# Performance work log

Measured on AMD Instinct MI355X. Metric: run time of the kernel, lower is better.

## Reference

```python
import jax, jax.numpy as jnp
import numpy as np

K = 32           # number of neighbors (init kwarg k)
NUM_CLASSES = 100  # fixed class vocabulary for jit-compatible bincount


def setup_inputs() -> dict:
    key = jax.random.key(0)
    k1, k2, k3 = jax.random.split(key, 3)
    X_test = jax.random.normal(k1, (2048, 512), dtype=jnp.float32)
    X_train = jax.random.normal(k2, (65536, 512), dtype=jnp.float32)
    y_train = jax.random.randint(k3, (65536,), 0, NUM_CLASSES, dtype=jnp.int32)
    return {"X_test": X_test, "X_train": X_train, "y_train": y_train}


def reference(X_test, X_train, y_train):
    # Pairwise euclidean distances via ||q||^2 - 2 q.t + ||t||^2  -> [Nq, Nt]
    q2 = jnp.sum(X_test * X_test, axis=1, keepdims=True)        # [Nq, 1]
    t2 = jnp.sum(X_train * X_train, axis=1)                      # [Nt]
    d2 = q2 - 2.0 * (X_test @ X_train.T) + t2[None, :]           # [Nq, Nt]
    dist = jnp.sqrt(jnp.maximum(d2, 0.0))
    # k smallest distances -> neighbor indices
    _, idx = jax.lax.top_k(-dist, K)                             # [Nq, K]
    neighbor_labels = y_train[idx]                               # [Nq, K]
    # bincount per query (vectorized) + argmax = majority vote
    counts = jnp.sum(jax.nn.one_hot(neighbor_labels, NUM_CLASSES, dtype=jnp.float32), axis=1)  # [Nq, C]
    y_pred = jnp.argmax(counts, axis=1).astype(jnp.int32)        # [Nq]
    return y_pred
```

## Files before the change

kernel.cpp:

```cpp
#include <hip/hip_runtime.h>
#include <hip/hip_bf16.h>
#include <stdint.h>

typedef unsigned long long u64;
typedef unsigned int u32;
typedef unsigned short u16;
typedef __attribute__((ext_vector_type(8))) short short8;
typedef __attribute__((ext_vector_type(16))) float float16;

#define NQ 2048
#define NT 65536
#define DIM 512
#define KNN 32
#define NC 100
#define NS 32

#define QT 32
#define SLICE (NT / NS)
#define TT 256
#define KK 16
#define FCAP 32

#define PQT 32
#define PTT 256
#define PSLICE 512
#define NTPRE 2048

#define MQT 128
#define MTT 128
#define MBK 32
#define MSLICE 2048
#define SCAP 16
#define NTILES 256

#define GCAP 4096

__global__ void norm_kernel(const float* __restrict__ X, float* __restrict__ out, int nrows) {
    int row = blockIdx.x * 4 + (threadIdx.x >> 6);
    int lane = threadIdx.x & 63;
    if (row >= nrows) return;
    const float4* p = (const float4*)(X + (size_t)row * DIM);
    float4 a = p[lane];
    float4 b = p[lane + 64];
    float s = a.x*a.x + a.y*a.y + a.z*a.z + a.w*a.w
            + b.x*b.x + b.y*b.y + b.z*b.z + b.w*b.w;
    #pragma unroll
    for (int off = 32; off > 0; off >>= 1) s += __shfl_down(s, off, 64);
    if (lane == 0) out[row] = s;
}

__global__ void split_kernel(const float* __restrict__ X, u16* __restrict__ H,
                             u16* __restrict__ L, int n4) {
    int i = blockIdx.x * 256 + threadIdx.x;
    if (i >= n4) return;
    float4 v = ((const float4*)X)[i];
    float f[4] = {v.x, v.y, v.z, v.w};
    u16 hh[4], ll[4];
    #pragma unroll
    for (int j = 0; j < 4; ++j) {
        union { __hip_bfloat16 b; u16 u; } cv;
        cv.b = __float2bfloat16(f[j]);
        hh[j] = cv.u;
        float hf = __bfloat162float(cv.b);
        cv.b = __float2bfloat16(f[j] - hf);
        ll[j] = cv.u;
    }
    ((ushort4*)H)[i] = make_ushort4(hh[0], hh[1], hh[2], hh[3]);
    ((ushort4*)L)[i] = make_ushort4(ll[0], ll[1], ll[2], ll[3]);
}

__launch_bounds__(256, 2)
__global__ void knn_pre(const float* __restrict__ Xq, const float* __restrict__ Xt,
                        const float* __restrict__ q2, const float* __restrict__ t2,
                        float* __restrict__ Dpre) {
    __shared__ float sQ[KK][PQT];
    __shared__ float sT[KK][PTT];

    const int tid = threadIdx.x;
    const int q0 = blockIdx.x * PQT;
    const int t0p = blockIdx.y * PSLICE;
    const int tq4 = (tid >> 5) * 4;
    const int tt4 = (tid & 31) * 4;
    const int pg = tid & 63;
    const int kg = tid >> 6;
    const int qp = tid & 31;
    const int kq = tid >> 5;

    float qq[4];
    #pragma unroll
    for (int i = 0; i < 4; ++i) qq[i] = q2[q0 + tq4 + i];

    #pragma unroll 1
    for (int chunk = 0; chunk < PSLICE / PTT; ++chunk) {
        const int tbase = t0p + chunk * PTT;
        float acc[4][8];
        #pragma unroll
        for (int i = 0; i < 4; ++i)
            #pragma unroll
            for (int j = 0; j < 8; ++j) acc[i][j] = 0.f;

        #pragma unroll 1
        for (int k0 = 0; k0 < DIM; k0 += KK) {
            __syncthreads();
            {
                const float* Tp = Xt + (size_t)(tbase + pg * 4) * DIM + k0 + kg * 4;
                float4 r0 = *(const float4*)(Tp);
                float4 r1 = *(const float4*)(Tp + DIM);
                float4 r2 = *(const float4*)(Tp + 2 * DIM);
                float4 r3 = *(const float4*)(Tp + 3 * DIM);
                *(float4*)&sT[kg * 4 + 0][pg * 4] = make_float4(r0.x, r1.x, r2.x, r3.x);
                *(float4*)&sT[kg * 4 + 1][pg * 4] = make_float4(r0.y, r1.y, r2.y, r3.y);
                *(float4*)&sT[kg * 4 + 2][pg * 4] = make_float4(r0.z, r1.z, r2.z, r3.z);
                *(float4*)&sT[kg * 4 + 3][pg * 4] = make_float4(r0.w, r1.w, r2.w, r3.w);
            }
            {
                float2 v = *(const float2*)(Xq + (size_t)(q0 + qp) * DIM + k0 + kq * 2);
                sQ[kq * 2 + 0][qp] = v.x;
                sQ[kq * 2 + 1][qp] = v.y;
            }
            __syncthreads();
            #pragma unroll
            for (int k = 0; k < KK; ++k) {
                float4 qv = *(const float4*)&sQ[k][tq4];
                float4 ta = *(const float4*)&sT[k][tt4];
                float4 tb = *(const float4*)&sT[k][128 + tt4];
                float qa[4] = {qv.x, qv.y, qv.z, qv.w};
                float tv[8] = {ta.x, ta.y, ta.z, ta.w, tb.x, tb.y, tb.z, tb.w};
                #pragma unroll
                for (int i = 0; i < 4; ++i)
                    #pragma unroll
                    for (int j = 0; j < 8; ++j)
                        acc[i][j] = fmaf(qa[i], tv[j], acc[i][j]);
            }
        }

        float t2v[8];
        #pragma unroll
        for (int j = 0; j < 4; ++j) {
            t2v[j]     = t2[tbase + tt4 + j];
            t2v[4 + j] = t2[tbase + 128 + tt4 + j];
        }
        #pragma unroll
        for (int i = 0; i < 4; ++i) {
            float4 lo, hi;
            lo.x = fmaxf(qq[i] - 2.f * acc[i][0] + t2v[0], 0.f);
            lo.y = fmaxf(qq[i] - 2.f * acc[i][1] + t2v[1], 0.f);
            lo.z = fmaxf(qq[i] - 2.f * acc[i][2] + t2v[2], 0.f);
            lo.w = fmaxf(qq[i] - 2.f * acc[i][3] + t2v[3], 0.f);
            hi.x = fmaxf(qq[i] - 2.f * acc[i][4] + t2v[4], 0.f);
            hi.y = fmaxf(qq[i] - 2.f * acc[i][5] + t2v[5], 0.f);
            hi.z = fmaxf(qq[i] - 2.f * acc[i][6] + t2v[6], 0.f);
            hi.w = fmaxf(qq[i] - 2.f * acc[i][7] + t2v[7], 0.f);
            *(float4*)&Dpre[(size_t)(q0 + tq4 + i) * NTPRE + tbase + tt4] = lo;
            *(float4*)&Dpre[(size_t)(q0 + tq4 + i) * NTPRE + tbase + 128 + tt4] = hi;
        }
    }
}

__launch_bounds__(64)
__global__ void seed_topk(const float* __restrict__ Dpre, u32* __restrict__ seed) {
    __shared__ u64 ll[64][KNN + 1];
    const int q = blockIdx.x;
    const int lane = threadIdx.x;
    #pragma unroll
    for (int j = 0; j <= KNN; ++j) ll[lane][j] = ~0ULL;
    const float* src = Dpre + (size_t)q * NTPRE;
    u64 kth = ~0ULL;
    for (int i = lane; i < NTPRE; i += 64) {
        u64 key = (u64)__float_as_uint(src[i]);
        if (key < kth) {
            int p = KNN - 1;
            while (p > 0 && ll[lane][p - 1] > key) { ll[lane][p] = ll[lane][p - 1]; --p; }
            ll[lane][p] = key;
            kth = ll[lane][KNN - 1];
        }
    }
    __syncthreads();
    int ptr = 0;
    u64 cur = ll[lane][0];
    u64 m = 0;
    for (int it = 0; it < KNN; ++it) {
        m = cur;
        #pragma unroll
        for (int off = 32; off > 0; off >>= 1) {
            u64 o = __shfl_xor(m, off, 64);
            m = (o < m) ? o : m;
        }
        u64 got = __ballot(cur == m);
        int w = __ffsll(got) - 1;
        if (lane == w) { ++ptr; cur = (ptr < KNN) ? ll[lane][ptr] : ~0ULL; }
    }
    if (lane == 0) seed[q] = (u32)m;
}

__device__ __forceinline__ void gld16(const void* g, void* l) {
    __builtin_amdgcn_global_load_lds(
        (const __attribute__((address_space(1))) u32*)g,
        (__attribute__((address_space(3))) u32*)l, 16, 0, 0);
}

__launch_bounds__(256, 4)
__global__ void gemm_filter(const u16* __restrict__ Qh, const u16* __restrict__ Ql,
                            const u16* __restrict__ Th, const u16* __restrict__ Tl,
                            const float* __restrict__ q2, const float* __restrict__ t2,
                            const u32* __restrict__ seed,
                            u32* __restrict__ gcnt, u64* __restrict__ glist) {
    __shared__ __align__(16) u16 tile[4][4096];
    __shared__ float sQ2L[128];
    __shared__ float sT2L[128];
    __shared__ u32 sSeed[128];

    const int tid = threadIdx.x;
    const int lane = tid & 63;
    const int wid = tid >> 6;
    const int q0g = blockIdx.x * 128;
    const int tb  = blockIdx.y * 128;
    const int m_off = (wid >> 1) * 64;
    const int n_off = (wid & 1) * 64;
    const int swz = ((lane >> 1) & 3) << 3;
    const int l4r = lane >> 2;
    const int l4c = (((lane & 3) ^ ((lane >> 3) & 3)) * 8);

    if (tid < 128) {
        sQ2L[tid] = q2[q0g + tid];
        sT2L[tid] = t2[tb + tid];
        sSeed[tid] = seed[q0g + tid] + 256u;
    }

    float16 acc[2][2];
    acc[0][0] = (float16)(0.0f); acc[0][1] = (float16)(0.0f);
    acc[1][0] = (float16)(0.0f); acc[1][1] = (float16)(0.0f);

    #pragma unroll 1
    for (int k0 = 0; k0 < DIM; k0 += MBK) {
        __syncthreads();
        #pragma unroll
        for (int u = 0; u < 4; ++u) {
            const u16* P = (u == 0) ? Qh : (u == 1) ? Ql : (u == 2) ? Th : Tl;
            const int rb = (u < 2) ? q0g : tb;
            #pragma unroll
            for (int j = 0; j < 2; ++j) {
                const int rg = j * 64 + wid * 16;
                gld16(P + (size_t)(rb + rg + l4r) * DIM + k0 + l4c,
                      (u16*)tile[u] + rg * 32);
            }
        }
        __syncthreads();

        #pragma unroll
        for (int s = 0; s < 2; ++s) {
            const int kb = (s * 16 + (lane >> 5) * 8) ^ swz;
            short8 ah[2], al[2], bh[2], bl[2];
            #pragma unroll
            for (int mi = 0; mi < 2; ++mi) {
                int row = m_off + mi * 32 + (lane & 31);
                ah[mi] = *(const short8*)(const void*)&tile[0][row * 32 + kb];
                al[mi] = *(const short8*)(const void*)&tile[1][row * 32 + kb];
            }
            #pragma unroll
            for (int nj = 0; nj < 2; ++nj) {
                int row = n_off + nj * 32 + (lane & 31);
                bh[nj] = *(const short8*)(const void*)&tile[2][row * 32 + kb];
                bl[nj] = *(const short8*)(const void*)&tile[3][row * 32 + kb];
            }
            #pragma unroll
            for (int mi = 0; mi < 2; ++mi)
                #pragma unroll
                for (int nj = 0; nj < 2; ++nj) {
                    acc[mi][nj] = __builtin_amdgcn_mfma_f32_32x32x16_bf16(ah[mi], bh[nj], acc[mi][nj], 0, 0, 0);
                    acc[mi][nj] = __builtin_amdgcn_mfma_f32_32x32x16_bf16(ah[mi], bl[nj], acc[mi][nj], 0, 0, 0);
                    acc[mi][nj] = __builtin_amdgcn_mfma_f32_32x32x16_bf16(al[mi], bh[nj], acc[mi][nj], 0, 0, 0);
                }
        }
    }

    #pragma unroll
    for (int mi = 0; mi < 2; ++mi)
        #pragma unroll
        for (int nj = 0; nj < 2; ++nj) {
            const int tcol_l = n_off + nj * 32 + (lane & 31);
            const float t2v = sT2L[tcol_l];
            #pragma unroll
            for (int r = 0; r < 16; ++r) {
                const int qrow_l = m_off + mi * 32 + (r & 3) + 8 * (r >> 2) + 4 * (lane >> 5);
                float d = fmaxf(sQ2L[qrow_l] - 2.0f * acc[mi][nj][r] + t2v, 0.0f);
                if (__float_as_uint(d) <= sSeed[qrow_l]) {
                    const int q = q0g + qrow_l;
                    u32 pos = atomicAdd(&gcnt[q], 1u);
                    if (pos < GCAP)
                        glist[(size_t)q * GCAP + pos] =
                            ((u64)__float_as_uint(d) << 16) | (u64)(u32)(tb + tcol_l);
                }
            }
        }
}

__launch_bounds__(64)
__global__ void knn_topk(const u64* __restrict__ glist, const u32* __restrict__ gcnt,
                         const int* __restrict__ y_train, int* __restrict__ out) {
    __shared__ u64 ll[64][KNN + 1];
    __shared__ u64 fin[KNN];
    __shared__ int counts[NC];
    const int q = blockIdx.x;
    const int lane = threadIdx.x;
    #pragma unroll
    for (int j = 0; j <= KNN; ++j) ll[lane][j] = ~0ULL;
    for (int i = lane; i < NC; i += 64) counts[i] = 0;
    u32 n = gcnt[q]; if (n > GCAP) n = GCAP;
    const u64* src = glist + (size_t)q * GCAP;
    u64 kth = ~0ULL;
    for (u32 i = lane; i < n; i += 64) {
        u64 key = src[i];
        if (key < kth) {
            int p = KNN - 1;
            while (p > 0 && ll[lane][p - 1] > key) { ll[lane][p] = ll[lane][p - 1]; --p; }
            ll[lane][p] = key;
            kth = ll[lane][KNN - 1];
        }
    }
    __syncthreads();
    int ptr = 0;
    u64 cur = ll[lane][0];
    for (int it = 0; it < KNN; ++it) {
        u64 m = cur;
        #pragma unroll
        for (int off = 32; off > 0; off >>= 1) {
            u64 o = __shfl_xor(m, off, 64);
            m = (o < m) ? o : m;
        }
        u64 got = __ballot(cur == m);
        int w = __ffsll(got) - 1;
        if (lane == 0) fin[it] = m;
        if (lane == w) { ++ptr; cur = (ptr < KNN) ? ll[lane][ptr] : ~0ULL; }
    }
    __syncthreads();
    if (lane < KNN) {
        int idx = (int)(fin[lane] & 0xFFFF);
        atomicAdd(&counts[y_train[idx]], 1);
    }
    __syncthreads();
    if (lane == 0) {
        int bestc = counts[0], bestl = 0;
        for (int c = 1; c < NC; ++c)
            if (counts[c] > bestc) { bestc = counts[c]; bestl = c; }
        out[q] = bestl;
    }
}


__launch_bounds__(256, 2)
__global__ void knn_prepass(const float* __restrict__ Xq, const float* __restrict__ Xt,
                            const float* __restrict__ q2, const float* __restrict__ t2,
                            u32* __restrict__ seed) {
    __shared__ float sQ[KK][PQT];
    __shared__ float sT[KK][PTT];
    __shared__ float sD[PQT][PTT + 1];
    __shared__ u32 topk[PQT][KNN + 1];

    const int tid = threadIdx.x;
    const int q0 = blockIdx.x * PQT;
    const int t0p = blockIdx.y * PSLICE;
    const int tq4 = (tid >> 5) * 4;
    const int tt4 = (tid & 31) * 4;
    const int pg = tid & 63;
    const int kg = tid >> 6;
    const int qp = tid & 31;
    const int kq = tid >> 5;

    for (int i = tid; i < PQT * (KNN + 1); i += 256) ((u32*)topk)[i] = 0xFFFFFFFFu;
    u32 kth = 0xFFFFFFFFu;

    float qq[4];
    #pragma unroll
    for (int i = 0; i < 4; ++i) qq[i] = q2[q0 + tq4 + i];

    #pragma unroll 1
    for (int chunk = 0; chunk < PSLICE / PTT; ++chunk) {
        const int tbase = t0p + chunk * PTT;
        float acc[4][8];
        #pragma unroll
        for (int i = 0; i < 4; ++i)
            #pragma unroll
            for (int j = 0; j < 8; ++j) acc[i][j] = 0.f;

        #pragma unroll 1
        for (int k0 = 0; k0 < DIM; k0 += KK) {
            __syncthreads();
            {
                const float* Tp = Xt + (size_t)(tbase + pg * 4) * DIM + k0 + kg * 4;
                float4 r0 = *(const float4*)(Tp);
                float4 r1 = *(const float4*)(Tp + DIM);
                float4 r2 = *(const float4*)(Tp + 2 * DIM);
                float4 r3 = *(const float4*)(Tp + 3 * DIM);
                *(float4*)&sT[kg * 4 + 0][pg * 4] = make_float4(r0.x, r1.x, r2.x, r3.x);
                *(float4*)&sT[kg * 4 + 1][pg * 4] = make_float4(r0.y, r1.y, r2.y, r3.y);
                *(float4*)&sT[kg * 4 + 2][pg * 4] = make_float4(r0.z, r1.z, r2.z, r3.z);
                *(float4*)&sT[kg * 4 + 3][pg * 4] = make_float4(r0.w, r1.w, r2.w, r3.w);
            }
            {
                float2 v = *(const float2*)(Xq + (size_t)(q0 + qp) * DIM + k0 + kq * 2);
                sQ[kq * 2 + 0][qp] = v.x;
                sQ[kq * 2 + 1][qp] = v.y;
            }
            __syncthreads();
            #pragma unroll
            for (int k = 0; k < KK; ++k) {
                float4 qv = *(const float4*)&sQ[k][tq4];
                float4 ta = *(const float4*)&sT[k][tt4];
                float4 tb = *(const float4*)&sT[k][128 + tt4];
                float qa[4] = {qv.x, qv.y, qv.z, qv.w};
                float tv[8] = {ta.x, ta.y, ta.z, ta.w, tb.x, tb.y, tb.z, tb.w};
                #pragma unroll
                for (int i = 0; i < 4; ++i)
                    #pragma unroll
                    for (int j = 0; j < 8; ++j)
                        acc[i][j] = fmaf(qa[i], tv[j], acc[i][j]);
            }
        }

        #pragma unroll
        for (int i = 0; i < 4; ++i)
            #pragma unroll
            for (int j = 0; j < 8; ++j) {
                int t = (j < 4) ? (tt4 + j) : (128 + tt4 + (j - 4));
                sD[tq4 + i][t] = fmaxf((qq[i] - 2.f * acc[i][j]) + t2[tbase + t], 0.f);
            }
        __syncthreads();

        if (tid < PQT) {
            for (int t = 0; t < PTT; ++t) {
                u32 d = __float_as_uint(sD[tid][t]);
                if (d < kth) {
                    int p = KNN - 1;
                    while (p > 0 && topk[tid][p - 1] > d) {
                        topk[tid][p] = topk[tid][p - 1];
                        --p;
                    }
                    topk[tid][p] = d;
                    kth = topk[tid][KNN - 1];
                }
            }
        }
    }
    if (tid < PQT) atomicMin(&seed[q0 + tid], kth);
}

__device__ __forceinline__ void stage_tile(const u16* __restrict__ Qh, const u16* __restrict__ Ql,
                                           const u16* __restrict__ Th, const u16* __restrict__ Tl,
                                           u16* base, int q0, int tb, int k0, int wid, int lane) {
    const int l4r = lane >> 2;
    const int l4c = (((lane & 3) ^ ((lane >> 3) & 3)) * 8);
    #pragma unroll
    for (int u = 0; u < 4; ++u) {
        const u16* P = (u == 0) ? Qh : (u == 1) ? Ql : (u == 2) ? Th : Tl;
        const int r0 = (u < 2) ? q0 : tb;
        const u16* g = P + (size_t)(r0 + wid * 16 + l4r) * DIM + k0 + l4c;
        gld16(g, base + u * 4096 + wid * 512);
    }
}

__launch_bounds__(512, 1)
__global__ void knn_mfma(const u16* __restrict__ Qh, const u16* __restrict__ Ql,
                         const u16* __restrict__ Th, const u16* __restrict__ Tl,
                         const float* __restrict__ q2, const float* __restrict__ t2,
                         const u32* __restrict__ seed, u64* __restrict__ cand) {
    __shared__ __align__(16) u16 tiles[3][16384];
    __shared__ u32 topkD[MQT][KNN + 1];
    __shared__ u16 topkI[MQT][KNN + 1];
    __shared__ u64 sbuf[MQT][SCAP];
    __shared__ u64 kth64[MQT];
    __shared__ u32 cnt[MQT];
    __shared__ float sQ2[MQT];
    __shared__ float sT2[MTT];
    __shared__ int againF;

    const int tid = threadIdx.x;
    const int lane = tid & 63;
    const int wid = tid >> 6;
    const int q0 = blockIdx.y * MQT;
    const int s0 = blockIdx.x * MSLICE;
    const int m_off = (wid >> 2) * 64;
    const int n_off = (wid & 3) * 32;
    const int swz = ((lane >> 1) & 3) << 3;

    for (int i = tid; i < MQT * (KNN + 1); i += 512) {
        ((u32*)topkD)[i] = 0xFFFFFFFFu;
        ((u16*)topkI)[i] = 0xFFFFu;
    }
    u64 seedkey = ~0ULL;
    if (tid < MQT) {
        seedkey = ((u64)seed[q0 + tid] + 1) << 16;
        kth64[tid] = seedkey;
        cnt[tid] = 0u;
        sQ2[tid] = q2[q0 + tid];
    }
    if (tid == 0) againF = 0;

    stage_tile(Qh, Ql, Th, Tl, tiles[0], q0, s0, 0, wid, lane);
    stage_tile(Qh, Ql, Th, Tl, tiles[1], q0, s0, MBK, wid, lane);
    __syncthreads();

    int cb = 0;
    #pragma unroll 1
    for (int chunk = 0; chunk < MSLICE / MTT; ++chunk) {
        const int tb = s0 + chunk * MTT;
        float16 acc[2];
        acc[0] = (float16)(0.0f);
        acc[1] = (float16)(0.0f);

        #pragma unroll 1
        for (int t = 0; t < DIM / MBK; ++t) {
            const int Tn = chunk * 16 + t + 2;
            const bool pf = (Tn < NTILES);
            if (pf) {
                int bn = cb + 2; if (bn >= 3) bn -= 3;
                stage_tile(Qh, Ql, Th, Tl, tiles[bn], q0,
                           s0 + (Tn >> 4) * MTT, (Tn & 15) * MBK, wid, lane);
            }
            const u16* sAh = tiles[cb];
            const u16* sAl = sAh + 4096;
            const u16* sBh = sAh + 8192;
            const u16* sBl = sAh + 12288;
            #pragma unroll
            for (int s = 0; s < 2; ++s) {
                const int kb = (s * 16 + (lane >> 5) * 8) ^ swz;
                short8 ah[2], al[2];
                #pragma unroll
                for (int mi = 0; mi < 2; ++mi) {
                    int row = m_off + mi * 32 + (lane & 31);
                    ah[mi] = *(const short8*)(const void*)&sAh[row * MBK + kb];
                    al[mi] = *(const short8*)(const void*)&sAl[row * MBK + kb];
                }
                int brow = n_off + (lane & 31);
                short8 bh = *(const short8*)(const void*)&sBh[brow * MBK + kb];
                short8 bl = *(const short8*)(const void*)&sBl[brow * MBK + kb];
                #pragma unroll
                for (int mi = 0; mi < 2; ++mi) {
                    acc[mi] = __builtin_amdgcn_mfma_f32_32x32x16_bf16(ah[mi], bh, acc[mi], 0, 0, 0);
                    acc[mi] = __builtin_amdgcn_mfma_f32_32x32x16_bf16(ah[mi], bl, acc[mi], 0, 0, 0);
                    acc[mi] = __builtin_amdgcn_mfma_f32_32x32x16_bf16(al[mi], bh, acc[mi], 0, 0, 0);
                }
            }
            if (pf) asm volatile("s_waitcnt vmcnt(4)" ::: "memory");
            else    asm volatile("s_waitcnt vmcnt(0)" ::: "memory");
            __builtin_amdgcn_s_barrier();
            __builtin_amdgcn_sched_barrier(0);
            ++cb; if (cb >= 3) cb = 0;
        }

        if (tid < MTT) sT2[tid] = t2[tb + tid];
        __syncthreads();
        const float t2r = sT2[n_off + (lane & 31)];
        const int tcol = n_off + (lane & 31);

        u32 mask = 0;
        for (;;) {
            #pragma unroll
            for (int mi = 0; mi < 2; ++mi) {
                #pragma unroll
                for (int r = 0; r < 16; ++r) {
                    const int bit = mi * 16 + r;
                    if ((mask >> bit) & 1) continue;
                    const int qrow = m_off + mi * 32 + (r & 3) + 8 * (r >> 2) + 4 * (lane >> 5);
                    float d = fmaxf(sQ2[qrow] - 2.0f * acc[mi][r] + t2r, 0.0f);
                    u64 key = ((u64)__float_as_uint(d) << 16) | (u64)(u32)(tb + tcol);
                    if (key < kth64[qrow]) {
                        u32 pos = atomicAdd(&cnt[qrow], 1u);
                        if (pos < SCAP) { sbuf[qrow][pos] = key; mask |= (1u << bit); }
                    }
                }
            }
            __syncthreads();
            if (tid < MQT) {
                u32 n = cnt[tid];
                u32 m = n < SCAP ? n : SCAP;
                for (u32 e = 0; e < m; ++e) {
                    u64 key = sbuf[tid][e];
                    u64 last = ((u64)topkD[tid][KNN - 1] << 16) | topkI[tid][KNN - 1];
                    if (key < last) {
                        int p = KNN - 1;
                        while (p > 0) {
                            u64 prev = ((u64)topkD[tid][p - 1] << 16) | topkI[tid][p - 1];
                            if (prev > key) {
                                topkD[tid][p] = topkD[tid][p - 1];
                                topkI[tid][p] = topkI[tid][p - 1];
                                --p;
                            } else break;
                        }
                        topkD[tid][p] = (u32)(key >> 16);
                        topkI[tid][p] = (u16)(key & 0xFFFF);
                    }
                }
                u64 last = ((u64)topkD[tid][KNN - 1] << 16) | topkI[tid][KNN - 1];
                kth64[tid] = last < seedkey ? last : seedkey;
                if (n > SCAP) againF = 1;
                cnt[tid] = 0u;
            }
            __syncthreads();
            int go = againF;
            __syncthreads();
            if (tid == 0) againF = 0;
            if (!go) break;
            __syncthreads();
        }
    }

    __syncthreads();
    for (int i = tid; i < MQT * KNN; i += 512) {
        int q = i >> 5, k = i & 31;
        u64 key = ((u64)topkD[q][k] << 16) | topkI[q][k];
        cand[((size_t)(q0 + q) * NS + blockIdx.x) * KNN + k] = key;
    }
}

__launch_bounds__(256, 4)
__global__ void knn_part(const float* __restrict__ Xq, const float* __restrict__ Xt,
                         const float* __restrict__ q2, const float* __restrict__ t2,
                         u64* __restrict__ cand) {
    __shared__ float sQ[KK][QT];
    __shared__ float sT[KK][TT];
    __shared__ u64 topk[QT][KNN];
    __shared__ u64 buf[QT][FCAP];
    __shared__ u64 kth64[QT];
    __shared__ u32 cnt[QT];
    __shared__ int againF;

    const int tid = threadIdx.x;
    const int q0 = blockIdx.x * QT;
    const int t0 = blockIdx.y * SLICE;
    const int tq4 = (tid >> 5) * 4;
    const int tt4 = (tid & 31) * 4;
    const int pg = tid & 63;
    const int kg = tid >> 6;
    const int qp = tid & 31;
    const int kq = tid >> 5;

    for (int i = tid; i < QT * KNN; i += 256) ((u64*)topk)[i] = ~0ULL;
    if (tid < QT) { kth64[tid] = ~0ULL; cnt[tid] = 0u; }
    if (tid == 0) againF = 0;

    float qq[4];
    #pragma unroll
    for (int i = 0; i < 4; ++i) qq[i] = q2[q0 + tq4 + i];

    #pragma unroll 1
    for (int chunk = 0; chunk < SLICE / TT; ++chunk) {
        const int tbase = t0 + chunk * TT;
        float acc[4][8];
        #pragma unroll
        for (int i = 0; i < 4; ++i)
            #pragma unroll
            for (int j = 0; j < 8; ++j) acc[i][j] = 0.f;

        #pragma unroll 1
        for (int k0 = 0; k0 < DIM; k0 += KK) {
            __syncthreads();
            {
                const float* Tp = Xt + (size_t)(tbase + pg * 4) * DIM + k0 + kg * 4;
                float4 r0 = *(const float4*)(Tp);
                float4 r1 = *(const float4*)(Tp + DIM);
                float4 r2 = *(const float4*)(Tp + 2 * DIM);
                float4 r3 = *(const float4*)(Tp + 3 * DIM);
                *(float4*)&sT[kg * 4 + 0][pg * 4] = make_float4(r0.x, r1.x, r2.x, r3.x);
                *(float4*)&sT[kg * 4 + 1][pg * 4] = make_float4(r0.y, r1.y, r2.y, r3.y);
                *(float4*)&sT[kg * 4 + 2][pg * 4] = make_float4(r0.z, r1.z, r2.z, r3.z);
                *(float4*)&sT[kg * 4 + 3][pg * 4] = make_float4(r0.w, r1.w, r2.w, r3.w);
            }
            {
                float2 v = *(const float2*)(Xq + (size_t)(q0 + qp) * DIM + k0 + kq * 2);
                sQ[kq * 2 + 0][qp] = v.x;
                sQ[kq * 2 + 1][qp] = v.y;
            }
            __syncthreads();
            #pragma unroll
            for (int k = 0; k < KK; ++k) {
                float4 qv = *(const float4*)&sQ[k][tq4];
                float4 ta = *(const float4*)&sT[k][tt4];
                float4 tb = *(const float4*)&sT[k][128 + tt4];
                float qa[4] = {qv.x, qv.y, qv.z, qv.w};
                float tv[8] = {ta.x, ta.y, ta.z, ta.w, tb.x, tb.y, tb.z, tb.w};
                #pragma unroll
                for (int i = 0; i < 4; ++i)
                    #pragma unroll
                    for (int j = 0; j < 8; ++j)
                        acc[i][j] = fmaf(qa[i], tv[j], acc[i][j]);
            }
        }

        float t2v[8];
        #pragma unroll
        for (int j = 0; j < 4; ++j) {
            t2v[j]     = t2[tbase + tt4 + j];
            t2v[4 + j] = t2[tbase + 128 + tt4 + j];
        }
        #pragma unroll
        for (int i = 0; i < 4; ++i)
            #pragma unroll
            for (int j = 0; j < 8; ++j)
                acc[i][j] = fmaxf((qq[i] - 2.f * acc[i][j]) + t2v[j], 0.f);

        unsigned mask = 0;
        for (;;) {
            u64 kv[4];
            #pragma unroll
            for (int i = 0; i < 4; ++i) kv[i] = kth64[tq4 + i];
            #pragma unroll
            for (int i = 0; i < 4; ++i) {
                #pragma unroll
                for (int j = 0; j < 8; ++j) {
                    unsigned b = 1u << (i * 8 + j);
                    if (mask & b) continue;
                    int tloc = (j < 4) ? (tt4 + j) : (128 + tt4 + (j - 4));
                    u64 key = ((u64)__float_as_uint(acc[i][j]) << 16) |
                              (u64)(unsigned)(tbase + tloc);
                    if (key < kv[i]) {
                        unsigned pos = atomicAdd(&cnt[tq4 + i], 1u);
                        if (pos < FCAP) { buf[tq4 + i][pos] = key; mask |= b; }
                    }
                }
            }
            __syncthreads();
            if (tid < QT) {
                unsigned n = cnt[tid];
                unsigned m = n < FCAP ? n : FCAP;
                for (unsigned e = 0; e < m; ++e) {
                    u64 key = buf[tid][e];
                    if (key < topk[tid][KNN - 1]) {
                        int p = KNN - 1;
                        while (p > 0 && topk[tid][p - 1] > key) {
                            topk[tid][p] = topk[tid][p - 1];
                            --p;
                        }
                        topk[tid][p] = key;
                    }
                }
                kth64[tid] = topk[tid][KNN - 1];
                if (n > FCAP) againF = 1;
                cnt[tid] = 0u;
            }
            __syncthreads();
            int go = againF;
            __syncthreads();
            if (tid == 0) againF = 0;
            if (!go) break;
            __syncthreads();
        }
    }

    __syncthreads();
    for (int i = tid; i < QT * KNN; i += 256) {
        int q = i >> 5, k = i & 31;
        cand[((size_t)(q0 + q) * NS + blockIdx.y) * KNN + k] = topk[q][k];
    }
}

__global__ void knn_merge(const u64* __restrict__ cand,
                          const int* __restrict__ y_train, int* __restrict__ out) {
    __shared__ u64 keys[NS * KNN];
    __shared__ u64 top[KNN];
    __shared__ int counts[NC];
    int q = blockIdx.x;
    for (int i = threadIdx.x; i < NS * KNN; i += 64)
        keys[i] = cand[(size_t)q * NS * KNN + i];
    for (int i = threadIdx.x; i < NC; i += 64) counts[i] = 0;
    if (threadIdx.x < KNN) top[threadIdx.x] = ~0ULL;
    __syncthreads();

    if (threadIdx.x == 0) {
        for (int s = 0; s < NS; ++s) {
            for (int j = 0; j < KNN; ++j) {
                u64 key = keys[s * KNN + j];
                if (key >= top[KNN - 1]) break;
                int p = KNN - 1;
                while (p > 0 && top[p - 1] > key) { top[p] = top[p - 1]; --p; }
                top[p] = key;
            }
        }
        for (int k = 0; k < KNN; ++k) {
            int idx = (int)(top[k] & 0xFFFF);
            counts[y_train[idx]]++;
        }
        int bestc = counts[0], bestl = 0;
        for (int c = 1; c < NC; ++c)
            if (counts[c] > bestc) { bestc = counts[c]; bestl = c; }
        out[q] = bestl;
    }
}

extern "C" void kernel_launch(void* const* d_in, const int* in_sizes, int n_in,
                              void* d_out, int out_size, void* d_ws, size_t ws_size,
                              hipStream_t stream) {
    const float* Xq = (const float*)d_in[0];
    const float* Xt = (const float*)d_in[1];
    const int*   y  = (const int*)d_in[2];
    int* out = (int*)d_out;

    float* t2 = (float*)d_ws;
    float* q2 = t2 + NT;
    u64* cand = (u64*)(q2 + NQ);
    u32* seed = (u32*)(cand + (size_t)NQ * NS * KNN);
    u16* Qh = (u16*)(seed + NQ);
    u16* Ql = Qh + (size_t)NQ * DIM;
    u16* Th = Ql + (size_t)NQ * DIM;
    u16* Tl = Th + (size_t)NT * DIM;
    u64* glist = (u64*)(Tl + (size_t)NT * DIM);
    u32* gcnt  = (u32*)(glist + (size_t)NQ * GCAP);
    float* Dpre = (float*)glist;

    const size_t need = (size_t)(NT + NQ) * 4
                      + (size_t)NQ * NS * KNN * 8
                      + (size_t)NQ * 4
                      + 2 * ((size_t)NQ * DIM + (size_t)NT * DIM) * 2;
    const bool use_mfma = ws_size >= need;
    const bool use_filter = ws_size >= need + (size_t)NQ * GCAP * 8 + (size_t)NQ * 4;

    norm_kernel<<<NT / 4, 256, 0, stream>>>(Xt, t2, NT);
    norm_kernel<<<NQ / 4, 256, 0, stream>>>(Xq, q2, NQ);
    if (use_mfma && use_filter) {
        split_kernel<<<(NQ * DIM / 4 + 255) / 256, 256, 0, stream>>>(Xq, Qh, Ql, NQ * DIM / 4);
        split_kernel<<<(NT * DIM / 4 + 255) / 256, 256, 0, stream>>>(Xt, Th, Tl, NT * DIM / 4);
        knn_pre<<<dim3(NQ / PQT, NTPRE / PSLICE), 256, 0, stream>>>(Xq, Xt, q2, t2, Dpre);
        seed_topk<<<NQ, 64, 0, stream>>>(Dpre, seed);
        hipMemsetAsync(gcnt, 0, NQ * sizeof(u32), stream);
        gemm_filter<<<dim3(NQ / 128, NT / 128), 256, 0, stream>>>(
            Qh, Ql, Th, Tl, q2, t2, seed, gcnt, glist);
        knn_topk<<<NQ, 64, 0, stream>>>(glist, gcnt, y, out);
    } else if (use_mfma) {
        hipMemsetAsync(seed, 0xFF, NQ * sizeof(u32), stream);
        split_kernel<<<(NQ * DIM / 4 + 255) / 256, 256, 0, stream>>>(Xq, Qh, Ql, NQ * DIM / 4);
        split_kernel<<<(NT * DIM / 4 + 255) / 256, 256, 0, stream>>>(Xt, Th, Tl, NT * DIM / 4);
        knn_prepass<<<dim3(NQ / PQT, NTPRE / PSLICE), 256, 0, stream>>>(Xq, Xt, q2, t2, seed);
        knn_mfma<<<dim3(NT / MSLICE, NQ / MQT), 512, 0, stream>>>(Qh, Ql, Th, Tl, q2, t2, seed, cand);
        knn_merge<<<NQ, 64, 0, stream>>>(cand, y, out);
    } else {
        knn_part<<<dim3(NQ / QT, NS), 256, 0, stream>>>(Xq, Xt, q2, t2, cand);
        knn_merge<<<NQ, 64, 0, stream>>>(cand, y, out);
    }
}
```

Baseline: 1.263 ms.

## Double-buffer gemm_filter LDS tiles and swizzle workgroup order for locality

Adds a second LDS tile buffer so the next K-slice is loaded with global_load_lds while MFMAs run on the current one, leaving one barrier per iteration. It also remaps the block index so consecutive workgroups share train tiles across query tiles, which should improve L2 reuse. The larger LDS footprint lowers launch bounds occupancy from 4 to 2 blocks per CU, which may reduce latency hiding.

```diff
diff --git a/kernel.cpp b/kernel.cpp
--- a/kernel.cpp
+++ b/kernel.cpp
@@ -199,13 +199,13 @@
         (__attribute__((address_space(3))) u32*)l, 16, 0, 0);
 }
 
-__launch_bounds__(256, 4)
+__launch_bounds__(256, 2)
 __global__ void gemm_filter(const u16* __restrict__ Qh, const u16* __restrict__ Ql,
                             const u16* __restrict__ Th, const u16* __restrict__ Tl,
                             const float* __restrict__ q2, const float* __restrict__ t2,
                             const u32* __restrict__ seed,
                             u32* __restrict__ gcnt, u64* __restrict__ glist) {
-    __shared__ __align__(16) u16 tile[4][4096];
+    __shared__ __align__(16) u16 tiles[2][4][4096];
     __shared__ float sQ2L[128];
     __shared__ float sT2L[128];
     __shared__ u32 sSeed[128];
@@ -213,8 +213,10 @@
     const int tid = threadIdx.x;
     const int lane = tid & 63;
     const int wid = tid >> 6;
-    const int q0g = blockIdx.x * 128;
-    const int tb  = blockIdx.y * 128;
+    const int bid = blockIdx.x + (int)(gridDim.x * blockIdx.y);
+    const int wg  = ((bid & 7) << 10) + (bid >> 3);
+    const int q0g = (wg & 15) * 128;
+    const int tb  = (wg >> 4) * 128;
     const int m_off = (wid >> 1) * 64;
     const int n_off = (wid & 1) * 64;
     const int swz = ((lane >> 1) & 3) << 3;
@@ -231,22 +233,33 @@
     acc[0][0] = (float16)(0.0f); acc[0][1] = (float16)(0.0f);
     acc[1][0] = (float16)(0.0f); acc[1][1] = (float16)(0.0f);
 
+    #define STAGE_TILE(BUF, K0)                                                        \
+        do {                                                                           \
+            _Pragma("unroll")                                                          \
+            for (int u = 0; u < 4; ++u) {                                              \
+                const u16* P = (u == 0) ? Qh : (u == 1) ? Ql : (u == 2) ? Th : Tl;     \
+                const int rb = (u < 2) ? q0g : tb;                                     \
+                _Pragma("unroll")                                                      \
+                for (int j = 0; j < 2; ++j) {                                          \
+                    const int rg = j * 64 + wid * 16;                                  \
+                    gld16(P + (size_t)(rb + rg + l4r) * DIM + (K0) + l4c,              \
+                          (u16*)tiles[BUF][u] + rg * 32);                              \
+                }                                                                      \
+            }                                                                          \
+        } while (0)
+
+    STAGE_TILE(0, 0);
+    __syncthreads();
+
+    int cur = 0;
     #pragma unroll 1
-    for (int k0 = 0; k0 < DIM; k0 += MBK) {
-        __syncthreads();
-        #pragma unroll
-        for (int u = 0; u < 4; ++u) {
-            const u16* P = (u == 0) ? Qh : (u == 1) ? Ql : (u == 2) ? Th : Tl;
-            const int rb = (u < 2) ? q0g : tb;
-            #pragma unroll
-            for (int j = 0; j < 2; ++j) {
-                const int rg = j * 64 + wid * 16;
-                gld16(P + (size_t)(rb + rg + l4r) * DIM + k0 + l4c,
-                      (u16*)tile[u] + rg * 32);
-            }
-        }
-        __syncthreads();
-
+    for (int t = 0; t < DIM / MBK; ++t) {
+        if (t + 1 < DIM / MBK) STAGE_TILE(cur ^ 1, (t + 1) * MBK);
+
+        const u16* pA0 = tiles[cur][0];
+        const u16* pA1 = tiles[cur][1];
+        const u16* pB0 = tiles[cur][2];
+        const u16* pB1 = tiles[cur][3];
         #pragma unroll
         for (int s = 0; s < 2; ++s) {
             const int kb = (s * 16 + (lane >> 5) * 8) ^ swz;
@@ -254,14 +267,14 @@
             #pragma unroll
             for (int mi = 0; mi < 2; ++mi) {
                 int row = m_off + mi * 32 + (lane & 31);
-                ah[mi] = *(const short8*)(const void*)&tile[0][row * 32 + kb];
-                al[mi] = *(const short8*)(const void*)&tile[1][row * 32 + kb];
+                ah[mi] = *(const short8*)(const void*)&pA0[row * 32 + kb];
+                al[mi] = *(const short8*)(const void*)&pA1[row * 32 + kb];
             }
             #pragma unroll
             for (int nj = 0; nj < 2; ++nj) {
                 int row = n_off + nj * 32 + (lane & 31);
-                bh[nj] = *(const short8*)(const void*)&tile[2][row * 32 + kb];
-                bl[nj] = *(const short8*)(const void*)&tile[3][row * 32 + kb];
+                bh[nj] = *(const short8*)(const void*)&pB0[row * 32 + kb];
+                bl[nj] = *(const short8*)(const void*)&pB1[row * 32 + kb];
             }
             #pragma unroll
             for (int mi = 0; mi < 2; ++mi)
@@ -272,7 +285,12 @@
                     acc[mi][nj] = __builtin_amdgcn_mfma_f32_32x32x16_bf16(al[mi], bh[nj], acc[mi][nj], 0, 0, 0);
                 }
         }
-    }
+        asm volatile("s_waitcnt vmcnt(0)" ::: "memory");
+        __builtin_amdgcn_s_barrier();
+        __builtin_amdgcn_sched_barrier(0);
+        cur ^= 1;
+    }
+    #undef STAGE_TILE
 
     #pragma unroll
     for (int mi = 0; mi < 2; ++mi)
```

Result: faster. 1.191 ms (-5.7%).

## Triple-buffer gemm_filter tiles with async prefetch, larger 128x256 block tiles

Applied to the files above, without the earlier changes.

Rewrites the gemm_filter main loop to use a three-stage LDS ring buffer filled by global_load_lds two k-steps ahead, replacing the two barriers per step with one barrier plus an explicit vmcnt wait. The block tile grows to 128x256 with 512 threads, and block indices are remapped so neighbouring blocks share training tiles for better L2 reuse. It also raises wave priority around the MFMA section. The aim is to hide global-load latency and cut sync overhead. In exchange, LDS use per block rises to about 144KB, allowing only one block per CU.

```diff
diff --git a/kernel.cpp b/kernel.cpp
--- a/kernel.cpp
+++ b/kernel.cpp
@@ -34,6 +34,8 @@
 #define NTILES 256
 
 #define GCAP 4096
+
+#define GBUF 24576
 
 __global__ void norm_kernel(const float* __restrict__ X, float* __restrict__ out, int nrows) {
     int row = blockIdx.x * 4 + (threadIdx.x >> 6);
@@ -199,54 +201,78 @@
         (__attribute__((address_space(3))) u32*)l, 16, 0, 0);
 }
 
-__launch_bounds__(256, 4)
+__launch_bounds__(512, 1)
 __global__ void gemm_filter(const u16* __restrict__ Qh, const u16* __restrict__ Ql,
                             const u16* __restrict__ Th, const u16* __restrict__ Tl,
                             const float* __restrict__ q2, const float* __restrict__ t2,
                             const u32* __restrict__ seed,
                             u32* __restrict__ gcnt, u64* __restrict__ glist) {
-    __shared__ __align__(16) u16 tile[4][4096];
+    __shared__ __align__(16) u16 tiles[3][GBUF];
     __shared__ float sQ2L[128];
-    __shared__ float sT2L[128];
+    __shared__ float sT2L[256];
     __shared__ u32 sSeed[128];
 
     const int tid = threadIdx.x;
     const int lane = tid & 63;
     const int wid = tid >> 6;
-    const int q0g = blockIdx.x * 128;
-    const int tb  = blockIdx.y * 128;
-    const int m_off = (wid >> 1) * 64;
-    const int n_off = (wid & 1) * 64;
+    const int bid = blockIdx.x + (int)(gridDim.x * blockIdx.y);
+    const int wg  = ((bid & 7) << 9) + (bid >> 3);
+    const int q0g = (wg & 15) * 128;
+    const int tb  = (wg >> 4) * 256;
+    const int m_off = (wid >> 2) * 64;
+    const int n_off = (wid & 3) * 64;
     const int swz = ((lane >> 1) & 3) << 3;
     const int l4r = lane >> 2;
     const int l4c = (((lane & 3) ^ ((lane >> 3) & 3)) * 8);
 
     if (tid < 128) {
         sQ2L[tid] = q2[q0g + tid];
-        sT2L[tid] = t2[tb + tid];
         sSeed[tid] = seed[q0g + tid] + 256u;
     }
+    if (tid < 256) sT2L[tid] = t2[tb + tid];
 
     float16 acc[2][2];
     acc[0][0] = (float16)(0.0f); acc[0][1] = (float16)(0.0f);
     acc[1][0] = (float16)(0.0f); acc[1][1] = (float16)(0.0f);
 
+    #define STAGE_TILE(BUF, K0)                                                         \
+        do {                                                                            \
+            _Pragma("unroll")                                                           \
+            for (int s6 = 0; s6 < 6; ++s6) {                                            \
+                const int ii = wid + s6 * 8;                                            \
+                const u16* P; int rb, off;                                              \
+                if (ii < 16) {                                                          \
+                    P = (ii < 8) ? Qh : Ql; rb = q0g;                                   \
+                    off = ((ii < 8) ? 0 : 4096) + (ii & 7) * 512;                       \
+                    rb += (ii & 7) * 16;                                                \
+                } else {                                                                \
+                    const int jj = ii - 16;                                             \
+                    P = (jj < 16) ? Th : Tl; rb = tb;                                   \
+                    off = 8192 + ((jj < 16) ? 0 : 8192) + (jj & 15) * 512;              \
+                    rb += (jj & 15) * 16;                                               \
+                }                                                                       \
+                gld16(P + (size_t)(rb + l4r) * DIM + (K0) + l4c,                        \
+                      (u16*)tiles[BUF] + off);                                          \
+            }                                                                           \
+        } while (0)
+
+    STAGE_TILE(0, 0);
+    STAGE_TILE(1, MBK);
+    __syncthreads();
+
+    int cb = 0;
     #pragma unroll 1
-    for (int k0 = 0; k0 < DIM; k0 += MBK) {
-        __syncthreads();
-        #pragma unroll
-        for (int u = 0; u < 4; ++u) {
-            const u16* P = (u == 0) ? Qh : (u == 1) ? Ql : (u == 2) ? Th : Tl;
-            const int rb = (u < 2) ? q0g : tb;
-            #pragma unroll
-            for (int j = 0; j < 2; ++j) {
-                const int rg = j * 64 + wid * 16;
-                gld16(P + (size_t)(rb + rg + l4r) * DIM + k0 + l4c,
-                      (u16*)tile[u] + rg * 32);
-            }
-        }
-        __syncthreads();
-
+    for (int t = 0; t < DIM / MBK; ++t) {
+        const bool pf = (t + 2 < DIM / MBK);
+        if (pf) {
+            int bn = cb + 2; if (bn >= 3) bn -= 3;
+            STAGE_TILE(bn, (t + 2) * MBK);
+        }
+        const u16* pAh = tiles[cb];
+        const u16* pAl = pAh + 4096;
+        const u16* pBh = pAh + 8192;
+        const u16* pBl = pAh + 16384;
+        __builtin_amdgcn_s_setprio(1);
         #pragma unroll
         for (int s = 0; s < 2; ++s) {
             const int kb = (s * 16 + (lane >> 5) * 8) ^ swz;
@@ -254,14 +280,14 @@
             #pragma unroll
             for (int mi = 0; mi < 2; ++mi) {
                 int row = m_off + mi * 32 + (lane & 31);
-                ah[mi] = *(const short8*)(const void*)&tile[0][row * 32 + kb];
-                al[mi] = *(const short8*)(const void*)&tile[1][row * 32 + kb];
+                ah[mi] = *(const short8*)(const void*)&pAh[row * 32 + kb];
+                al[mi] = *(const short8*)(const void*)&pAl[row * 32 + kb];
             }
             #pragma unroll
             for (int nj = 0; nj < 2; ++nj) {
                 int row = n_off + nj * 32 + (lane & 31);
-                bh[nj] = *(const short8*)(const void*)&tile[2][row * 32 + kb];
-                bl[nj] = *(const short8*)(const void*)&tile[3][row * 32 + kb];
+                bh[nj] = *(const short8*)(const void*)&pBh[row * 32 + kb];
+                bl[nj] = *(const short8*)(const void*)&pBl[row * 32 + kb];
             }
             #pragma unroll
             for (int mi = 0; mi < 2; ++mi)
@@ -272,7 +298,14 @@
                     acc[mi][nj] = __builtin_amdgcn_mfma_f32_32x32x16_bf16(al[mi], bh[nj], acc[mi][nj], 0, 0, 0);
                 }
         }
-    }
+        __builtin_amdgcn_s_setprio(0);
+        if (pf) asm volatile("s_waitcnt vmcnt(6)" ::: "memory");
+        else    asm volatile("s_waitcnt vmcnt(0)" ::: "memory");
+        __builtin_amdgcn_s_barrier();
+        __builtin_amdgcn_sched_barrier(0);
+        ++cb; if (cb >= 3) cb = 0;
+    }
+    #undef STAGE_TILE
 
     #pragma unroll
     for (int mi = 0; mi < 2; ++mi)
@@ -822,7 +855,7 @@
         knn_pre<<<dim3(NQ / PQT, NTPRE / PSLICE), 256, 0, stream>>>(Xq, Xt, q2, t2, Dpre);
         seed_topk<<<NQ, 64, 0, stream>>>(Dpre, seed);
         hipMemsetAsync(gcnt, 0, NQ * sizeof(u32), stream);
-        gemm_filter<<<dim3(NQ / 128, NT / 128), 256, 0, stream>>>(
+        gemm_filter<<<dim3(NQ / 128, NT / 256), 512, 0, stream>>>(
             Qh, Ql, Th, Tl, q2, t2, seed, gcnt, glist);
         knn_topk<<<NQ, 64, 0, stream>>>(glist, gcnt, y, out);
     } else if (use_mfma) {
```

Result: faster. 1.230 ms (-2.6%).
